# Kernel tuning notes

Hardware: AMD Instinct MI355X
Metric: run time of the kernel (lower is better)

The kernel has to match this reference:

```python
import jax, jax.numpy as jnp
import numpy as np

N_NODES = 100000
NUM_GRAPHS = 128
HEADS = 4
NEG_SLOPE = 0.2  # PyG GATConv default


def _gat_conv(x, src, dst, W, att_s, att_d, bias, heads, n_nodes, concat):
    # x: [N, F_in]; W: [F_in, heads*C]; att_s/att_d: [heads, C]; bias: [heads*C] or [C]
    h = (x @ W).reshape(n_nodes, heads, -1)            # [N, H, C]
    a_s = jnp.einsum('nhc,hc->nh', h, att_s)            # [N, H]
    a_d = jnp.einsum('nhc,hc->nh', h, att_d)            # [N, H]
    e = jax.nn.leaky_relu(a_s[src] + a_d[dst], NEG_SLOPE)  # [E, H]
    m = jax.ops.segment_max(e, dst, num_segments=n_nodes)  # [N, H]
    ex = jnp.exp(e - m[dst])                                # [E, H]
    denom = jax.ops.segment_sum(ex, dst, num_segments=n_nodes)  # [N, H]
    alpha = ex / (denom[dst] + 1e-16)                       # [E, H]
    msg = h[src] * alpha[:, :, None]                        # [E, H, C]
    out = jax.ops.segment_sum(msg, dst, num_segments=n_nodes)  # [N, H, C]
    if concat:
        out = out.reshape(n_nodes, -1)                      # [N, H*C]
    else:
        out = out.mean(axis=1)                              # [N, C]
    return out + bias


def setup_inputs() -> dict:
    key = jax.random.key(0)
    ks = jax.random.split(key, 12)
    in_c, hid, out_c, H = 128, 32, 10, HEADS
    E = 1600000
    x = jax.random.normal(ks[0], (N_NODES, in_c), dtype=jnp.float32)
    edge_index = jax.random.randint(ks[1], (2, E), 0, N_NODES, dtype=jnp.int32)
    batch = jnp.sort(jax.random.randint(ks[2], (N_NODES,), 0, NUM_GRAPHS, dtype=jnp.int32))
    s1 = 1.0 / np.sqrt(in_c)
    s2 = 1.0 / np.sqrt(hid * H)
    W1 = jax.random.uniform(ks[3], (in_c, H * hid), jnp.float32, -s1, s1)
    att_src1 = jax.random.uniform(ks[4], (H, hid), jnp.float32, -s1, s1)
    att_dst1 = jax.random.uniform(ks[5], (H, hid), jnp.float32, -s1, s1)
    b1 = jnp.zeros((H * hid,), jnp.float32)
    W2 = jax.random.uniform(ks[6], (H * hid, out_c), jnp.float32, -s2, s2)
    att_src2 = jax.random.uniform(ks[7], (1, out_c), jnp.float32, -s2, s2)
    att_dst2 = jax.random.uniform(ks[8], (1, out_c), jnp.float32, -s2, s2)
    b2 = jnp.zeros((out_c,), jnp.float32)
    return {"x": x, "W1": W1, "att_src1": att_src1, "att_dst1": att_dst1, "b1": b1,
            "W2": W2, "att_src2": att_src2, "att_dst2": att_dst2, "b2": b2,
            "edge_index": edge_index, "batch": batch}


def reference(x, W1, att_src1, att_dst1, b1, W2, att_src2, att_dst2, b2, edge_index, batch):
    n = x.shape[0]
    loops = jnp.arange(n, dtype=edge_index.dtype)
    src = jnp.concatenate([edge_index[0], loops])  # add_self_loops=True
    dst = jnp.concatenate([edge_index[1], loops])
    h = jax.nn.elu(_gat_conv(x, src, dst, W1, att_src1, att_dst1, b1, HEADS, n, concat=True))
    h = jax.nn.elu(_gat_conv(h, src, dst, W2, att_src2, att_dst2, b2, 1, n, concat=False))
    # global mean pool over graphs
    sums = jax.ops.segment_sum(h, batch, num_segments=NUM_GRAPHS)
    cnts = jax.ops.segment_sum(jnp.ones((n,), h.dtype), batch, num_segments=NUM_GRAPHS)
    pooled = sums / jnp.maximum(cnts, 1.0)[:, None]
    return jax.nn.log_softmax(pooled, axis=1)
```

## Files before the change

kernel.cpp:

```cpp
#include <hip/hip_runtime.h>
#include <cstdint>
#include <cstddef>

#define LRELU(x) fmaxf((x), 0.2f*(x))

typedef float v2f __attribute__((ext_vector_type(2)));
typedef __attribute__((ext_vector_type(8))) short short8;
typedef __attribute__((ext_vector_type(4))) float f32x4;

__device__ inline unsigned short f2bf(float f) {
  unsigned u = __float_as_uint(f);
  u += 0x8000u;
  return (unsigned short)(u >> 16);
}
__device__ inline float bflo(unsigned u) { return __uint_as_float(u << 16); }
__device__ inline float bfhi(unsigned u) { return __uint_as_float(u & 0xffff0000u); }

__global__ __launch_bounds__(256) void k_gemm1p(const float* __restrict__ x,
                                               const float* __restrict__ W1,
                                               const float* __restrict__ atts1,
                                               const float* __restrict__ attd1,
                                               int* __restrict__ h1f8,
                                               float* __restrict__ a_s, float* __restrict__ a_d,
                                               float* __restrict__ poolcnt,
                                               int N, int gemmBlocks,
                                               const int* __restrict__ ei, int E, int Etot,
                                               int Nd, int cap,
                                               int* __restrict__ bcnt, int2* __restrict__ bdata) {
  __shared__ short Wt[128*136];
  int t = threadIdx.x;

  if (blockIdx.x >= gemmBlocks) {
    int* hist = (int*)Wt;
    int* cur  = ((int*)Wt) + 256;
    if (t < 256) hist[t] = 0;
    __syncthreads();
    int base = (blockIdx.x - gemmBlocks)*4096;
    int dreg[16]; short sreg[16];
    #pragma unroll
    for (int k = 0; k < 16; ++k) {
      int e = base + k*256 + t;
      int s = -1, d = 0;
      if (e < Etot) {
        d = (e < E) ? ei[E + e] : (e - E);
        s = d / Nd;
        atomicAdd(&hist[s], 1);
      }
      dreg[k] = d; sreg[k] = (short)s;
    }
    __syncthreads();
    if (t < 256) cur[t] = atomicAdd(&bcnt[t], hist[t]);
    __syncthreads();
    #pragma unroll
    for (int k = 0; k < 16; ++k) {
      int s = sreg[k];
      if (s < 0) continue;
      int e = base + k*256 + t;
      int src = (e < E) ? ei[e] : dreg[k];
      int pos = atomicAdd(&cur[s], 1);
      if (pos < cap) bdata[(size_t)s*cap + pos] = make_int2(src, dreg[k]);
    }
    return;
  }

  int gid = blockIdx.x*256 + t;
  if (gid < 1408) poolcnt[gid] = 0.f;

  {
    int n = t & 127, half = t >> 7;
    for (int kk0 = 0; kk0 < 64; kk0 += 4) {
      short v0 = (short)f2bf(W1[(half*64 + kk0 + 0)*128 + n]);
      short v1 = (short)f2bf(W1[(half*64 + kk0 + 1)*128 + n]);
      short v2 = (short)f2bf(W1[(half*64 + kk0 + 2)*128 + n]);
      short v3 = (short)f2bf(W1[(half*64 + kk0 + 3)*128 + n]);
      *(short4*)(&Wt[n*136 + half*64 + kk0]) = make_short4(v0, v1, v2, v3);
    }
  }
  __syncthreads();

  int w = t >> 6, l = t & 63;
  int n0 = blockIdx.x*64 + w*16;
  int mrow = l & 15, q = l >> 4;
  int nrow = n0 + mrow; if (nrow >= N) nrow = N - 1;
  const float4* xrow = (const float4*)(x + (size_t)nrow*128);
  f32x4 acc[8];
  #pragma unroll
  for (int i = 0; i < 8; ++i) acc[i] = (f32x4){0.f, 0.f, 0.f, 0.f};
  #pragma unroll
  for (int kc = 0; kc < 4; ++kc) {
    float4 xa = xrow[kc*8 + q*2];
    float4 xb = xrow[kc*8 + q*2 + 1];
    short8 afr;
    afr[0] = (short)f2bf(xa.x); afr[1] = (short)f2bf(xa.y);
    afr[2] = (short)f2bf(xa.z); afr[3] = (short)f2bf(xa.w);
    afr[4] = (short)f2bf(xb.x); afr[5] = (short)f2bf(xb.y);
    afr[6] = (short)f2bf(xb.z); afr[7] = (short)f2bf(xb.w);
    #pragma unroll
    for (int ti = 0; ti < 8; ++ti) {
      short8 bfr = *(const short8*)(&Wt[(ti*16 + mrow)*136 + kc*32 + q*8]);
      acc[ti] = __builtin_amdgcn_mfma_f32_16x16x32_bf16(afr, bfr, acc[ti], 0, 0, 0);
    }
  }
  __syncthreads();
  float* hs = ((float*)Wt) + w*2112;
  #pragma unroll
  for (int ti = 0; ti < 8; ++ti) {
    #pragma unroll
    for (int r = 0; r < 4; ++r)
      hs[(q*4 + r)*132 + ti*16 + mrow] = acc[ti][r];
  }
  {
    int nd = l >> 2, head = l & 3;
    int ndg = n0 + nd;
    const float4* hr  = (const float4*)(hs + nd*132 + head*32);
    const float4* asv = (const float4*)(atts1 + head*32);
    const float4* adv = (const float4*)(attd1 + head*32);
    float ps = 0.f, pd = 0.f;
    int pk[8];
    #pragma unroll
    for (int j = 0; j < 8; ++j) {
      float4 v = hr[j];
      float4 sa = asv[j], da = adv[j];
      ps += v.x*sa.x + v.y*sa.y + v.z*sa.z + v.w*sa.w;
      pd += v.x*da.x + v.y*da.y + v.z*da.z + v.w*da.w;
      int p = __builtin_amdgcn_cvt_pk_fp8_f32(v.x, v.y, 0, false);
      p = __builtin_amdgcn_cvt_pk_fp8_f32(v.z, v.w, p, true);
      pk[j] = p;
    }
    if (ndg < N) {
      int4* dst = (int4*)(h1f8 + (size_t)ndg*32 + head*8);
      dst[0] = make_int4(pk[0], pk[1], pk[2], pk[3]);
      dst[1] = make_int4(pk[4], pk[5], pk[6], pk[7]);
      a_s[ndg*4 + head] = ps;
      a_d[ndg*4 + head] = pd;
    }
  }
}

__global__ __launch_bounds__(256) void k_scatter_b(const int2* __restrict__ bdata,
    const int* __restrict__ bcnt, int Nd, int cap, int N,
    int* __restrict__ deg, int* __restrict__ srcs) {
  __shared__ int lcnt[512];
  int t = threadIdx.x;
  int s = blockIdx.x;
  int lo = s*Nd;
  for (int i = t; i < Nd; i += 256) lcnt[i] = 0;
  __syncthreads();
  int cnt = bcnt[s]; if (cnt > cap) cnt = cap;
  const int2* bp = bdata + (size_t)s*cap;
  for (int i = t; i < cnt; i += 256) {
    int2 ev = bp[i];
    int slot = atomicAdd(&lcnt[ev.y - lo], 1);
    if (slot < 64) srcs[((size_t)ev.y << 6) + slot] = ev.x;
  }
  __syncthreads();
  for (int i = t; i < Nd && lo + i < N; i += 256) deg[lo + i] = lcnt[i];
}

__global__ __launch_bounds__(256, 8) void k_agg1g2(const int* __restrict__ deg,
    const int* __restrict__ srcs, const float* __restrict__ a_s,
    const float* __restrict__ a_d, const int* __restrict__ h1f8,
    const float* __restrict__ b1, const float* __restrict__ W2,
    const float* __restrict__ atts2, const float* __restrict__ attd2,
    unsigned short* __restrict__ gb, float* __restrict__ a_s2, float* __restrict__ a_d2,
    int N) {
  __shared__ float W2t[1280];
  __shared__ float att2s[20];
  int t = threadIdx.x;
  for (int f = t; f < 1280; f += 256) {
    int c = f >> 7, k = f & 127;
    W2t[f] = W2[k*10 + c];
  }
  if (t < 20) att2s[t] = (t < 10) ? atts2[t] : attd2[t - 10];
  __syncthreads();

  int dst = (blockIdx.x*256 + t) >> 5;
  if (dst >= N) return;
  int l = t & 31;
  int sub = l & 15;
  int epair = l >> 4;
  int myhead = sub >> 2;
  int eh = l & 3;
  int ee = l >> 2;
  int beg = dst << 6;
  int dcnt = deg[dst]; if (dcnt > 64) dcnt = 64;
  int end = beg + dcnt;
  float4 ad4 = ((const float4*)a_d)[dst];
  float adh = (eh==0) ? ad4.x : (eh==1) ? ad4.y : (eh==2) ? ad4.z : ad4.w;
  float wacc = 0.f;
  v2f accA = (v2f){0.f,0.f}, accB = (v2f){0.f,0.f};
  v2f accC = (v2f){0.f,0.f}, accD = (v2f){0.f,0.f};
  const float4* as4p = (const float4*)a_s;
  const int2* h2p = (const int2*)h1f8;

  for (int g = beg; g < end; g += 32) {
    int gl = g + l;
    int se_all = srcs[gl < end ? gl : end - 1];
    int sec0 = __shfl(se_all, 0*8 + ee, 32);
    int sec1 = __shfl(se_all, 1*8 + ee, 32);
    int sec2 = __shfl(se_all, 2*8 + ee, 32);
    int sec3 = __shfl(se_all, 3*8 + ee, 32);
    float4 g0 = as4p[sec0];
    float4 g1 = as4p[sec1];
    float4 g2 = as4p[sec2];
    float4 g3 = as4p[sec3];
    float ash0 = (eh==0) ? g0.x : (eh==1) ? g0.y : (eh==2) ? g0.z : g0.w;
    float ash1 = (eh==0) ? g1.x : (eh==1) ? g1.y : (eh==2) ? g1.z : g1.w;
    float ash2 = (eh==0) ? g2.x : (eh==1) ? g2.y : (eh==2) ? g2.z : g2.w;
    float ash3 = (eh==0) ? g3.x : (eh==1) ? g3.y : (eh==2) ? g3.z : g3.w;
    float ashs[4] = {ash0, ash1, ash2, ash3};
    int nrem = end - g;
    #pragma unroll
    for (int c = 0; c < 4; ++c) {
      if (c*8 >= nrem) break;
      int rm = nrem - c*8 - 1;
      float w = __expf(LRELU(ashs[c] + adh));
      if (ee > rm) w = 0.f;
      wacc += w;
      int2 u[4]; float we[4];
      #pragma unroll
      for (int k = 0; k < 4; ++k) {
        int e = k*2 + epair;
        int s_e = __shfl(se_all, c*8 + e, 32);
        we[k]   = __shfl(w, e*4 + myhead, 32);
        u[k] = h2p[(size_t)s_e*16 + sub];
      }
      #pragma unroll
      for (int k = 0; k < 4; ++k) {
        v2f lo0 = __builtin_amdgcn_cvt_pk_f32_fp8(u[k].x, false);
        v2f hi0 = __builtin_amdgcn_cvt_pk_f32_fp8(u[k].x, true);
        v2f lo1 = __builtin_amdgcn_cvt_pk_f32_fp8(u[k].y, false);
        v2f hi1 = __builtin_amdgcn_cvt_pk_f32_fp8(u[k].y, true);
        v2f wv = (v2f){we[k], we[k]};
        accA += wv*lo0; accB += wv*hi0; accC += wv*lo1; accD += wv*hi1;
      }
    }
  }
  wacc += __shfl_xor(wacc, 4, 32);
  wacc += __shfl_xor(wacc, 8, 32);
  wacc += __shfl_xor(wacc, 16, 32);
  float denom = __shfl(wacc, myhead, 32);

  accA.x += __shfl_xor(accA.x, 16, 32); accA.y += __shfl_xor(accA.y, 16, 32);
  accB.x += __shfl_xor(accB.x, 16, 32); accB.y += __shfl_xor(accB.y, 16, 32);
  accC.x += __shfl_xor(accC.x, 16, 32); accC.y += __shfl_xor(accC.y, 16, 32);
  accD.x += __shfl_xor(accD.x, 16, 32); accD.y += __shfl_xor(accD.y, 16, 32);

  float inv = 1.0f / (denom + 1e-16f);
  float4 b1a = ((const float4*)b1)[sub*2];
  float4 b1b = ((const float4*)b1)[sub*2 + 1];
  float h0 = accA.x*inv + b1a.x; h0 = h0 > 0.f ? h0 : __expf(h0) - 1.0f;
  float h1 = accA.y*inv + b1a.y; h1 = h1 > 0.f ? h1 : __expf(h1) - 1.0f;
  float h2 = accB.x*inv + b1a.z; h2 = h2 > 0.f ? h2 : __expf(h2) - 1.0f;
  float h3 = accB.y*inv + b1a.w; h3 = h3 > 0.f ? h3 : __expf(h3) - 1.0f;
  float h4 = accC.x*inv + b1b.x; h4 = h4 > 0.f ? h4 : __expf(h4) - 1.0f;
  float h5 = accC.y*inv + b1b.y; h5 = h5 > 0.f ? h5 : __expf(h5) - 1.0f;
  float h6 = accD.x*inv + b1b.z; h6 = h6 > 0.f ? h6 : __expf(h6) - 1.0f;
  float h7 = accD.y*inv + b1b.w; h7 = h7 > 0.f ? h7 : __expf(h7) - 1.0f;

  const float4* W2t4 = (const float4*)W2t;
  float pc[5];
  #pragma unroll
  for (int cq = 0; cq < 5; ++cq) {
    int c = epair*5 + cq;
    float4 w0 = W2t4[c*32 + sub*2];
    float4 w1 = W2t4[c*32 + sub*2 + 1];
    pc[cq] = h0*w0.x + h1*w0.y + h2*w0.z + h3*w0.w
           + h4*w1.x + h5*w1.y + h6*w1.z + h7*w1.w;
  }
  #pragma unroll
  for (int off = 8; off > 0; off >>= 1) {
    #pragma unroll
    for (int cq = 0; cq < 5; ++cq)
      pc[cq] += __shfl_xor(pc[cq], off, 32);
  }
  if (sub < 5) {
    float val = pc[0];
    #pragma unroll
    for (int cq = 1; cq < 5; ++cq) val = (sub == cq) ? pc[cq] : val;
    gb[(size_t)dst*16 + epair*5 + sub] = f2bf(val);
  }
  float asH = 0.f, advH = 0.f;
  #pragma unroll
  for (int cq = 0; cq < 5; ++cq) {
    asH  += pc[cq]*att2s[epair*5 + cq];
    advH += pc[cq]*att2s[10 + epair*5 + cq];
  }
  asH  += __shfl_xor(asH, 16, 32);
  advH += __shfl_xor(advH, 16, 32);
  if (l == 0) {
    a_s2[dst] = asH;
    a_d2[dst] = advH;
  }
}

__global__ __launch_bounds__(256) void k_agg2f(const int* __restrict__ deg,
    const int* __restrict__ srcs, const float* __restrict__ a_s,
    const float* __restrict__ a_d, const unsigned short* __restrict__ gb,
    const float* __restrict__ b2, const int* __restrict__ batch,
    float* __restrict__ pooled, float* __restrict__ cnt, int N) {
  __shared__ float lp[4*10];
  __shared__ float lc[4];
  __shared__ int b0s;
  int t = threadIdx.x;
  int dst = (blockIdx.x*256 + t) >> 4;
  int l = t & 15;
  if (t < 40) lp[t] = 0.f;
  if (t < 4) lc[t] = 0.f;
  if (t == 0) {
    int d0 = (blockIdx.x*256) >> 4;
    if (d0 > N - 1) d0 = N - 1;
    b0s = batch[d0];
  }
  __syncthreads();
  int b0 = b0s;
  bool valid = (dst < N);
  float o = 0.f;
  int b = 0;
  if (valid) {
    int beg = dst << 6;
    int dcnt = deg[dst]; if (dcnt > 64) dcnt = 64;
    int end = beg + dcnt;
    float ad = a_d[dst];
    float acc[10] = {};
    float denom = 0.f;
    const uint4* g4 = (const uint4*)gb;
    const unsigned* gu = (const unsigned*)gb;
    int j = beg + l;
    if (j < end) {
      int s0 = srcs[j];
      int j1 = j + 16;
      int s1 = (j1 < end) ? srcs[j1] : s0;
      float av0 = a_s[s0];
      uint4  A0 = g4[(size_t)s0*2];
      unsigned B0 = gu[(size_t)s0*8 + 4];
      for (; j < end; j += 16) {
        float av1 = a_s[s1];
        uint4  A1 = g4[(size_t)s1*2];
        unsigned B1 = gu[(size_t)s1*8 + 4];
        int j2 = j + 32;
        int s2 = (j2 < end) ? srcs[j2] : s1;
        float w = __expf(LRELU(av0 + ad));
        denom += w;
        acc[0] += w*bflo(A0.x); acc[1] += w*bfhi(A0.x);
        acc[2] += w*bflo(A0.y); acc[3] += w*bfhi(A0.y);
        acc[4] += w*bflo(A0.z); acc[5] += w*bfhi(A0.z);
        acc[6] += w*bflo(A0.w); acc[7] += w*bfhi(A0.w);
        acc[8] += w*bflo(B0);   acc[9] += w*bfhi(B0);
        av0 = av1; A0 = A1; B0 = B1; s1 = s2;
      }
    }
    #pragma unroll
    for (int off = 8; off > 0; off >>= 1) {
      denom += __shfl_xor(denom, off, 16);
      #pragma unroll
      for (int c = 0; c < 10; ++c) acc[c] += __shfl_xor(acc[c], off, 16);
    }
    b = batch[dst];
    if (l < 10) {
      o = acc[l] / (denom + 1e-16f) + b2[l];
      o = o > 0.f ? o : __expf(o) - 1.0f;
    }
  }
  if (valid) {
    int bl = b - b0;
    if (l < 10) {
      if (bl < 4) atomicAdd(&lp[bl*10 + l], o);
      else atomicAdd(&pooled[b*10 + l], o);
    }
    if (l == 0) {
      if (bl < 4) atomicAdd(&lc[bl], 1.0f);
      else atomicAdd(&cnt[b], 1.0f);
    }
  }
  __syncthreads();
  if (t < 40) {
    int bl = t / 10, c = t - bl*10;
    int bb = b0 + bl;
    if (bb < 128 && lp[t] != 0.f) atomicAdd(&pooled[bb*10 + c], lp[t]);
  }
  if (t < 4) {
    int bb = b0 + t;
    if (bb < 128 && lc[t] != 0.f) atomicAdd(&cnt[bb], lc[t]);
  }
}

__global__ __launch_bounds__(128) void k_softmax(const float* __restrict__ pooled,
    const float* __restrict__ cnt, float* __restrict__ out) {
  int t = threadIdx.x;
  float inv = 1.0f / fmaxf(cnt[t], 1.0f);
  float v[10], m = -1e30f;
  #pragma unroll
  for (int c = 0; c < 10; ++c) { v[c] = pooled[t*10 + c] * inv; m = fmaxf(m, v[c]); }
  float s = 0.f;
  #pragma unroll
  for (int c = 0; c < 10; ++c) s += __expf(v[c] - m);
  float ls = logf(s) + m;
  #pragma unroll
  for (int c = 0; c < 10; ++c) out[t*10 + c] = v[c] - ls;
}

extern "C" void kernel_launch(void* const* d_in, const int* in_sizes, int n_in,
                              void* d_out, int out_size, void* d_ws, size_t ws_size,
                              hipStream_t stream) {
  const float* x     = (const float*)d_in[0];
  const float* W1    = (const float*)d_in[1];
  const float* atts1 = (const float*)d_in[2];
  const float* attd1 = (const float*)d_in[3];
  const float* b1    = (const float*)d_in[4];
  const float* W2    = (const float*)d_in[5];
  const float* atts2 = (const float*)d_in[6];
  const float* attd2 = (const float*)d_in[7];
  const float* b2    = (const float*)d_in[8];
  const int*   ei    = (const int*)d_in[9];
  const int*   batch = (const int*)d_in[10];
  int N = in_sizes[10];
  int E = in_sizes[9] / 2;
  int Etot = E + N;
  int NB = 256;
  int Nd  = (N + NB - 1) / NB;
  int cap = (Etot / NB) + 2048;

  char* base = (char*)d_ws;
  size_t off = 0;
  auto allocB = [&](size_t bytes) { void* p = (void*)(base + off); off += (bytes + 63) & ~size_t(63); return p; };

  int*   h1f8   = (int*)allocB((size_t)N*32*sizeof(int));
  float* a_s1   = (float*)allocB((size_t)N*4*sizeof(float));
  float* a_d1   = (float*)allocB((size_t)N*4*sizeof(float));
  unsigned short* gb = (unsigned short*)allocB((size_t)N*16*sizeof(unsigned short));
  float* a_s2   = (float*)allocB((size_t)N*sizeof(float));
  float* a_d2   = (float*)allocB((size_t)N*sizeof(float));
  float* poolcnt= (float*)allocB(1408*sizeof(float));
  int* bcnt   = (int*)allocB(NB*sizeof(int));
  int* deg    = (int*)allocB((size_t)N*sizeof(int));
  int* srcs   = (int*)allocB((size_t)N*64*sizeof(int));
  int2* bdata = (int2*)allocB((size_t)NB*cap*sizeof(int2));

  float* pooled = poolcnt;
  float* cnt    = poolcnt + 1280;
  int gemmBlocks = (N + 63)/64;
  int partBlocks = (Etot + 4095)/4096;

  hipMemsetAsync(bcnt, 0, NB*sizeof(int), stream);
  k_gemm1p<<<dim3(gemmBlocks + partBlocks), dim3(256), 0, stream>>>(
      x, W1, atts1, attd1, h1f8, a_s1, a_d1, poolcnt, N, gemmBlocks,
      ei, E, Etot, Nd, cap, bcnt, bdata);
  k_scatter_b<<<dim3(NB), dim3(256), 0, stream>>>(bdata, bcnt, Nd, cap, N, deg, srcs);
  k_agg1g2<<<dim3((N*32 + 255)/256), dim3(256), 0, stream>>>(deg, srcs, a_s1, a_d1, h1f8,
                                                             b1, W2, atts2, attd2,
                                                             gb, a_s2, a_d2, N);
  k_agg2f<<<dim3((N*16 + 255)/256), dim3(256), 0, stream>>>(deg, srcs, a_s2, a_d2, gb,
                                                            b2, batch, pooled, cnt, N);
  k_softmax<<<dim3(1), dim3(128), 0, stream>>>(pooled, cnt, (float*)d_out);
}
```

Measured before the change: 275.6 us.

## Fold attention vectors into GEMM weights and make GEMM blocks persistent

The attention dot products are folded algebraically into the layer-1 weight matrix as 8 extra bf16 columns, so a_s/a_d come straight out of an extra MFMA tile. The MFMA operands are swapped so results are written directly from registers, removing the shared-memory staging pass and its barrier. GEMM blocks become persistent (capped at 512) and loop over tiles. The W2 shared layout in the aggregation kernel is padded to reduce bank conflicts. Computing the attention logits from bf16-rounded folded weights adds some precision loss.

```diff
diff --git a/kernel.cpp b/kernel.cpp
--- a/kernel.cpp
+++ b/kernel.cpp
@@ -23,11 +23,11 @@
                                                int* __restrict__ h1f8,
                                                float* __restrict__ a_s, float* __restrict__ a_d,
                                                float* __restrict__ poolcnt,
-                                               int N, int gemmBlocks,
+                                               int N, int nTiles, int gemmBlocks,
                                                const int* __restrict__ ei, int E, int Etot,
                                                int Nd, int cap,
                                                int* __restrict__ bcnt, int2* __restrict__ bdata) {
-  __shared__ short Wt[128*136];
+  __shared__ short Wt[144*136];
   int t = threadIdx.x;
 
   if (blockIdx.x >= gemmBlocks) {
@@ -77,62 +77,62 @@
     }
   }
   __syncthreads();
+  {
+    int k = t & 127;
+    int jb = (t >> 7)*4;
+    for (int j = jb; j < jb + 4; ++j) {
+      int h = j & 3;
+      const float* att = (j < 4) ? (atts1 + h*32) : (attd1 + h*32);
+      float s = 0.f;
+      #pragma unroll
+      for (int c = 0; c < 32; ++c) {
+        unsigned short us = (unsigned short)Wt[(h*32 + c)*136 + k];
+        s += bflo(us) * att[c];
+      }
+      Wt[(128 + j)*136 + k] = (short)f2bf(s);
+    }
+    int rr = t >> 7;
+    for (int jj = rr; jj < 8; jj += 2) Wt[(136 + jj)*136 + k] = 0;
+  }
+  __syncthreads();
 
   int w = t >> 6, l = t & 63;
-  int n0 = blockIdx.x*64 + w*16;
   int mrow = l & 15, q = l >> 4;
-  int nrow = n0 + mrow; if (nrow >= N) nrow = N - 1;
-  const float4* xrow = (const float4*)(x + (size_t)nrow*128);
-  f32x4 acc[8];
-  #pragma unroll
-  for (int i = 0; i < 8; ++i) acc[i] = (f32x4){0.f, 0.f, 0.f, 0.f};
-  #pragma unroll
-  for (int kc = 0; kc < 4; ++kc) {
-    float4 xa = xrow[kc*8 + q*2];
-    float4 xb = xrow[kc*8 + q*2 + 1];
-    short8 afr;
-    afr[0] = (short)f2bf(xa.x); afr[1] = (short)f2bf(xa.y);
-    afr[2] = (short)f2bf(xa.z); afr[3] = (short)f2bf(xa.w);
-    afr[4] = (short)f2bf(xb.x); afr[5] = (short)f2bf(xb.y);
-    afr[6] = (short)f2bf(xb.z); afr[7] = (short)f2bf(xb.w);
-    #pragma unroll
-    for (int ti = 0; ti < 8; ++ti) {
-      short8 bfr = *(const short8*)(&Wt[(ti*16 + mrow)*136 + kc*32 + q*8]);
-      acc[ti] = __builtin_amdgcn_mfma_f32_16x16x32_bf16(afr, bfr, acc[ti], 0, 0, 0);
-    }
-  }
-  __syncthreads();
-  float* hs = ((float*)Wt) + w*2112;
-  #pragma unroll
-  for (int ti = 0; ti < 8; ++ti) {
-    #pragma unroll
-    for (int r = 0; r < 4; ++r)
-      hs[(q*4 + r)*132 + ti*16 + mrow] = acc[ti][r];
-  }
-  {
-    int nd = l >> 2, head = l & 3;
-    int ndg = n0 + nd;
-    const float4* hr  = (const float4*)(hs + nd*132 + head*32);
-    const float4* asv = (const float4*)(atts1 + head*32);
-    const float4* adv = (const float4*)(attd1 + head*32);
-    float ps = 0.f, pd = 0.f;
-    int pk[8];
-    #pragma unroll
-    for (int j = 0; j < 8; ++j) {
-      float4 v = hr[j];
-      float4 sa = asv[j], da = adv[j];
-      ps += v.x*sa.x + v.y*sa.y + v.z*sa.z + v.w*sa.w;
-      pd += v.x*da.x + v.y*da.y + v.z*da.z + v.w*da.w;
-      int p = __builtin_amdgcn_cvt_pk_fp8_f32(v.x, v.y, 0, false);
-      p = __builtin_amdgcn_cvt_pk_fp8_f32(v.z, v.w, p, true);
-      pk[j] = p;
-    }
-    if (ndg < N) {
-      int4* dst = (int4*)(h1f8 + (size_t)ndg*32 + head*8);
-      dst[0] = make_int4(pk[0], pk[1], pk[2], pk[3]);
-      dst[1] = make_int4(pk[4], pk[5], pk[6], pk[7]);
-      a_s[ndg*4 + head] = ps;
-      a_d[ndg*4 + head] = pd;
+
+  for (int tile = blockIdx.x; tile < nTiles; tile += gemmBlocks) {
+    int n0t = tile*64 + w*16;
+    int node = n0t + mrow;
+    int nrow = node < N ? node : N - 1;
+    const float4* xrow = (const float4*)(x + (size_t)nrow*128);
+    f32x4 acc[9];
+    #pragma unroll
+    for (int i = 0; i < 9; ++i) acc[i] = (f32x4){0.f, 0.f, 0.f, 0.f};
+    #pragma unroll
+    for (int kc = 0; kc < 4; ++kc) {
+      float4 xa = xrow[kc*8 + q*2];
+      float4 xb = xrow[kc*8 + q*2 + 1];
+      short8 afr;
+      afr[0] = (short)f2bf(xa.x); afr[1] = (short)f2bf(xa.y);
+      afr[2] = (short)f2bf(xa.z); afr[3] = (short)f2bf(xa.w);
+      afr[4] = (short)f2bf(xb.x); afr[5] = (short)f2bf(xb.y);
+      afr[6] = (short)f2bf(xb.z); afr[7] = (short)f2bf(xb.w);
+      #pragma unroll
+      for (int ti = 0; ti < 9; ++ti) {
+        short8 bfr = *(const short8*)(&Wt[(ti*16 + mrow)*136 + kc*32 + q*8]);
+        acc[ti] = __builtin_amdgcn_mfma_f32_16x16x32_bf16(bfr, afr, acc[ti], 0, 0, 0);
+      }
+    }
+    if (node < N) {
+      #pragma unroll
+      for (int ti = 0; ti < 8; ++ti) {
+        int p = __builtin_amdgcn_cvt_pk_fp8_f32(acc[ti][0], acc[ti][1], 0, false);
+        p = __builtin_amdgcn_cvt_pk_fp8_f32(acc[ti][2], acc[ti][3], p, true);
+        h1f8[(size_t)node*32 + ti*4 + q] = p;
+      }
+      if (q == 0)
+        *(float4*)(a_s + (size_t)node*4) = make_float4(acc[8][0], acc[8][1], acc[8][2], acc[8][3]);
+      if (q == 1)
+        *(float4*)(a_d + (size_t)node*4) = make_float4(acc[8][0], acc[8][1], acc[8][2], acc[8][3]);
     }
   }
 }
@@ -164,12 +164,16 @@
     const float* __restrict__ atts2, const float* __restrict__ attd2,
     unsigned short* __restrict__ gb, float* __restrict__ a_s2, float* __restrict__ a_d2,
     int N) {
-  __shared__ float W2t[1280];
+  __shared__ float W2s[1344];
   __shared__ float att2s[20];
   int t = threadIdx.x;
-  for (int f = t; f < 1280; f += 256) {
-    int c = f >> 7, k = f & 127;
-    W2t[f] = W2[k*10 + c];
+  for (int e = t; e < 320; e += 256) {
+    int sub = e / 20, rem = e - sub*20;
+    int c = rem >> 1, j = rem & 1;
+    int k0 = sub*8 + j*4;
+    ((float4*)W2s)[sub*21 + c*2 + j] =
+        make_float4(W2[(k0+0)*10 + c], W2[(k0+1)*10 + c],
+                    W2[(k0+2)*10 + c], W2[(k0+3)*10 + c]);
   }
   if (t < 20) att2s[t] = (t < 10) ? atts2[t] : attd2[t - 10];
   __syncthreads();
@@ -258,13 +262,13 @@
   float h6 = accD.x*inv + b1b.z; h6 = h6 > 0.f ? h6 : __expf(h6) - 1.0f;
   float h7 = accD.y*inv + b1b.w; h7 = h7 > 0.f ? h7 : __expf(h7) - 1.0f;
 
-  const float4* W2t4 = (const float4*)W2t;
+  const float4* W2s4 = (const float4*)W2s;
   float pc[5];
   #pragma unroll
   for (int cq = 0; cq < 5; ++cq) {
     int c = epair*5 + cq;
-    float4 w0 = W2t4[c*32 + sub*2];
-    float4 w1 = W2t4[c*32 + sub*2 + 1];
+    float4 w0 = W2s4[sub*21 + c*2];
+    float4 w1 = W2s4[sub*21 + c*2 + 1];
     pc[cq] = h0*w0.x + h1*w0.y + h2*w0.z + h3*w0.w
            + h4*w1.x + h5*w1.y + h6*w1.z + h7*w1.w;
   }
@@ -439,12 +443,14 @@
 
   float* pooled = poolcnt;
   float* cnt    = poolcnt + 1280;
-  int gemmBlocks = (N + 63)/64;
+  int nTiles = (N + 63)/64;
+  int gemmBlocks = 512;
+  if (gemmBlocks > nTiles) gemmBlocks = nTiles;
   int partBlocks = (Etot + 4095)/4096;
 
   hipMemsetAsync(bcnt, 0, NB*sizeof(int), stream);
   k_gemm1p<<<dim3(gemmBlocks + partBlocks), dim3(256), 0, stream>>>(
-      x, W1, atts1, attd1, h1f8, a_s1, a_d1, poolcnt, N, gemmBlocks,
+      x, W1, atts1, attd1, h1f8, a_s1, a_d1, poolcnt, N, nTiles, gemmBlocks,
       ei, E, Etot, Nd, cap, bcnt, bdata);
   k_scatter_b<<<dim3(NB), dim3(256), 0, stream>>>(bdata, bcnt, Nd, cap, N, deg, srcs);
   k_agg1g2<<<dim3((N*32 + 255)/256), dim3(256), 0, stream>>>(deg, srcs, a_s1, a_d1, h1f8,
```

Measured after the change: 269.5 us. -2.2%, faster.
